# Kernel tuning notes

Measured on AMD Instinct MI355X. Metric: run time of the kernel, lower is better.

Reference implementation:

```python
import jax, jax.numpy as jnp
import numpy as np

TAU = 0.1
EPS_FREQ = 1e-06
EPS_DENOM = 1e-12


def _l2norm(x, eps=1e-12):
    # matches F.normalize(p=2, dim=-1)
    n = jnp.linalg.norm(x, axis=-1, keepdims=True)
    return x / jnp.maximum(n, eps)


def setup_inputs() -> dict:
    key = jax.random.key(0)
    k1, k2, k3, k4, k5 = jax.random.split(key, 5)
    N, D, C = 4096, 128, 64
    return {
        "protos": jax.random.normal(k1, (C, D), dtype=jnp.float32),
        "proj2": jax.random.normal(k2, (N, D), dtype=jnp.float32),
        "target2": jax.random.randint(k3, (N,), 0, C, dtype=jnp.int64),
        "proj3": jax.random.normal(k4, (N, D), dtype=jnp.float32),
        "target3": jax.random.randint(k5, (N,), 0, C, dtype=jnp.int64),
    }


def reference(protos, proj2, target2, proj3, target3):
    feats = _l2norm(jnp.concatenate([proj2, proj3], axis=0))        # [M, D]
    labels = jnp.concatenate([target2, target3], axis=0)             # [M]
    protos_n = _l2norm(protos)                                       # [C, D]
    M = feats.shape[0]
    C = protos_n.shape[0]

    sim = jnp.matmul(feats, feats.T) / TAU                           # [M, M]
    proto_sim = jnp.matmul(feats, protos_n.T) / TAU                  # [M, C]

    eye = jnp.eye(M, dtype=bool)
    exp_sim = jnp.where(eye, 0.0, jnp.exp(sim))                      # diag masked to -inf -> exp 0
    exp_proto = jnp.exp(proto_sim)

    match = labels[:, None] == labels[None, :]                       # [M, M]
    numer_region = jnp.sum(exp_sim * match, axis=1)                  # [M]
    numer_proto = jnp.take_along_axis(exp_proto, labels[:, None], axis=1)[:, 0]
    numer = numer_region + numer_proto

    # bincount(labels ++ arange(C)) == per-class count + 1
    cls_freq = jnp.zeros((C,), dtype=jnp.float32).at[labels].add(1.0) + 1.0 + EPS_FREQ
    feat_w = cls_freq[labels]                                        # [M], per-row weight

    denom_region = jnp.sum(exp_sim, axis=1) / feat_w                 # row-constant weight; diag already 0
    denom_proto = jnp.sum(exp_proto / cls_freq[None, :], axis=1)
    denom = denom_region + denom_proto

    loss = -jnp.log(numer / (denom + EPS_DENOM))
    return jnp.mean(loss)
```

## Files before the change

kernel.cpp:

```cpp
#include <hip/hip_runtime.h>
#include <math.h>
#include <stdint.h>

#define D    128
#define CCLS 64
#define CH   8

typedef _Float16 f16x8 __attribute__((ext_vector_type(8)));
typedef float    f32x4 __attribute__((ext_vector_type(4)));

__device__ __forceinline__ float wave_reduce_sum(float v) {
    #pragma unroll
    for (int off = 32; off > 0; off >>= 1) v += __shfl_xor(v, off, 64);
    return v;
}

__device__ __forceinline__ void gload_lds16(const void* g, void* l) {
    __builtin_amdgcn_global_load_lds(
        (const __attribute__((address_space(1))) uint32_t*)g,
        (__attribute__((address_space(3))) uint32_t*)l, 16, 0, 0);
}
__device__ __forceinline__ void gload_lds4(const void* g, void* l) {
    __builtin_amdgcn_global_load_lds(
        (const __attribute__((address_space(1))) uint32_t*)g,
        (__attribute__((address_space(3))) uint32_t*)l, 4, 0, 0);
}

__global__ void norm_kernel(const float* __restrict__ protos,
                            const float* __restrict__ proj2,
                            const float* __restrict__ proj3,
                            const int* __restrict__ t2, const int* __restrict__ t3,
                            _Float16* __restrict__ ftile, int* __restrict__ labs,
                            float* __restrict__ cls_freq, float* __restrict__ loss_sum,
                            int N, int M) {
    const float SCL = 3.8017368953f;
    int w = threadIdx.x >> 6;
    int lane = threadIdx.x & 63;
    int row = blockIdx.x * (blockDim.x >> 6) + w;
    const int MT = M + 128;

    if (blockIdx.x == 0) {
        __shared__ int h[CCLS];
        int t = threadIdx.x;
        if (t < CCLS) h[t] = 0;
        if (t == 0) loss_sum[0] = 0.f;
        __syncthreads();
        for (int i = t; i < M; i += blockDim.x) {
            int lab = (i < N) ? t2[i] : t3[i - N];
            atomicAdd(&h[lab], 1);
        }
        __syncthreads();
        if (t < CCLS) cls_freq[t] = (float)h[t] + 1.0f + 1e-6f;
    }

    if (row < MT) {
        const float* src = nullptr;
        if (row < M)             src = (row < N) ? proj2 + (size_t)row * D
                                                 : proj3 + (size_t)(row - N) * D;
        else if (row < M + CCLS) src = protos + (size_t)(row - M) * D;
        float2 v = {0.f, 0.f};
        if (src) v = ((const float2*)src)[lane];
        float ss = wave_reduce_sum(v.x * v.x + v.y * v.y);
        float scale = src ? SCL / fmaxf(sqrtf(ss), 1e-12f) : 0.f;
        _Float16 h0 = (_Float16)(v.x * scale), h1 = (_Float16)(v.y * scale);
        int k0 = 2 * lane;
        size_t off = ((size_t)(row >> 4) * 16 + (k0 >> 3)) * 128 + (row & 15) * 8 + (k0 & 7);
        ftile[off] = h0; ftile[off + 1] = h1;
        if (row < M && lane == 0)
            labs[row] = (row < N) ? t2[row] : t3[row - N];
    }
}

__global__ __launch_bounds__(512, 4)
void sim_kernel(const _Float16* __restrict__ ftile,
                const int* __restrict__ labs,
                const float* __restrict__ cls_freq,
                float* __restrict__ nPart, float* __restrict__ dPart,
                float* __restrict__ rp, int M) {
    __shared__ _Float16 sbuf[2][8320];

    const int panel = blockIdx.x;
    const int chunk = blockIdx.y;
    const int t = threadIdx.x;
    const int w = t >> 6, lane = t & 63;
    const int g = lane >> 4, li = lane & 15;
    const int lo = g * 128 + li * 8;
    const int rtA = panel * 8 + w;
    const int nS = (M / 64) / CH;
    const int sBase = chunk * nS;
    const int row = panel * 128 + 16 * w + li;
    const int rl = labs[row];

    f16x8 a[4];
    #pragma unroll
    for (int kt = 0; kt < 4; ++kt)
        a[kt] = *(const f16x8*)(ftile + (size_t)rtA * 2048 + kt * 512 + lo);

    float rn = 0.f, rd = 0.f;

    #define STAGE(buf, s)                                                        \
        {                                                                        \
            const char* bsrc_ = (const char*)ftile + (size_t)(s) * 16384;        \
            char* dst_ = (char*)&sbuf[(buf)][0];                                 \
            _Pragma("unroll")                                                    \
            for (int q = 0; q < 2; ++q) {                                        \
                int j_ = w * 2 + q;                                              \
                gload_lds16(bsrc_ + (size_t)j_ * 1024 + lane * 16,               \
                            dst_ + (size_t)j_ * 1024);                           \
            }                                                                    \
            if (w == 0)                                                          \
                gload_lds4((const char*)labs + (size_t)(s) * 256 + lane * 4,     \
                           dst_ + 16384);                                        \
        }

    STAGE(0, sBase);
    __syncthreads();
    int cur = 0;

    const int diagS = 2 * panel + (w >> 2);
    const int nDiag = w & 3;

    for (int si = 0; si < nS; ++si) {
        const int s = sBase + si;
        if (si + 1 < nS) STAGE(cur ^ 1, sBase + si + 1);

        const _Float16* Bl = &sbuf[cur][0];
        const int* clabL = (const int*)&sbuf[cur][8192];

        f32x4 acc1[4];
        #pragma unroll
        for (int n = 0; n < 4; ++n)
            #pragma unroll
            for (int r = 0; r < 4; ++r) acc1[n][r] = 0.f;

        #pragma unroll
        for (int kt = 0; kt < 4; ++kt) {
            f16x8 b[4];
            #pragma unroll
            for (int n = 0; n < 4; ++n)
                b[n] = *(const f16x8*)(Bl + n * 2048 + kt * 512 + lo);
            #pragma unroll
            for (int n = 0; n < 4; ++n)
                acc1[n] = __builtin_amdgcn_mfma_f32_16x16x32_f16(b[n], a[kt], acc1[n], 0, 0, 0);
        }

        if (s == diagS) {
            #pragma unroll
            for (int n = 0; n < 4; ++n)
                #pragma unroll
                for (int r = 0; r < 4; ++r)
                    acc1[n][r] = (n == nDiag && 4 * g + r == li) ? -1e5f : acc1[n][r];
        }

        #pragma unroll
        for (int n = 0; n < 4; ++n) {
            int4 c4 = *(const int4*)(clabL + 16 * n + 4 * g);
            float e0 = __builtin_amdgcn_exp2f(acc1[n][0]);
            float e1 = __builtin_amdgcn_exp2f(acc1[n][1]);
            float e2 = __builtin_amdgcn_exp2f(acc1[n][2]);
            float e3 = __builtin_amdgcn_exp2f(acc1[n][3]);
            rd += e0 + e1 + e2 + e3;
            rn += (c4.x == rl) ? e0 : 0.f;
            rn += (c4.y == rl) ? e1 : 0.f;
            rn += (c4.z == rl) ? e2 : 0.f;
            rn += (c4.w == rl) ? e3 : 0.f;
        }

        __syncthreads();
        cur ^= 1;
    }

    float rpacc = 0.f;
    if (chunk == 0) {
        const int rbp = M >> 4;
        f32x4 accp[4];
        #pragma unroll
        for (int n = 0; n < 4; ++n)
            #pragma unroll
            for (int r = 0; r < 4; ++r) accp[n][r] = 0.f;
        #pragma unroll
        for (int kt = 0; kt < 4; ++kt) {
            f16x8 b[4];
            #pragma unroll
            for (int n = 0; n < 4; ++n)
                b[n] = *(const f16x8*)(ftile + (size_t)(rbp + n) * 2048 + kt * 512 + lo);
            #pragma unroll
            for (int n = 0; n < 4; ++n)
                accp[n] = __builtin_amdgcn_mfma_f32_16x16x32_f16(b[n], a[kt], accp[n], 0, 0, 0);
        }
        #pragma unroll
        for (int n = 0; n < 4; ++n) {
            f32x4 fr = *(const f32x4*)(cls_freq + 16 * n + 4 * g);
            const int c0 = 16 * n + 4 * g;
            float e0 = __builtin_amdgcn_exp2f(accp[n][0]);
            float e1 = __builtin_amdgcn_exp2f(accp[n][1]);
            float e2 = __builtin_amdgcn_exp2f(accp[n][2]);
            float e3 = __builtin_amdgcn_exp2f(accp[n][3]);
            rpacc += e0 / fr[0] + e1 / fr[1] + e2 / fr[2] + e3 / fr[3];
            rn += (c0 + 0 == rl) ? e0 : 0.f;
            rn += (c0 + 1 == rl) ? e1 : 0.f;
            rn += (c0 + 2 == rl) ? e2 : 0.f;
            rn += (c0 + 3 == rl) ? e3 : 0.f;
        }
    }

    rn += __shfl_xor(rn, 16, 64); rn += __shfl_xor(rn, 32, 64);
    rd += __shfl_xor(rd, 16, 64); rd += __shfl_xor(rd, 32, 64);
    if (chunk == 0) {
        rpacc += __shfl_xor(rpacc, 16, 64); rpacc += __shfl_xor(rpacc, 32, 64);
    }
    if (lane < 16) {
        nPart[(size_t)chunk * M + row] = rn;
        dPart[(size_t)chunk * M + row] = rd;
        if (chunk == 0) rp[row] = rpacc;
    }
}

__global__ void fin_kernel(const int* __restrict__ labs,
                           const float* __restrict__ cls_freq,
                           const float* __restrict__ nPart,
                           const float* __restrict__ dPart,
                           const float* __restrict__ rp,
                           float* __restrict__ loss_sum, int M) {
    int i = blockIdx.x * blockDim.x + threadIdx.x;
    float l = 0.f;
    if (i < M) {
        float rnT = 0.f, rdT = 0.f;
        #pragma unroll
        for (int ch = 0; ch < CH; ++ch) {
            rnT += nPart[(size_t)ch * M + i];
            rdT += dPart[(size_t)ch * M + i];
        }
        float denom = rdT / cls_freq[labs[i]] + rp[i];
        l = logf(denom + 1e-12f) - logf(rnT);
    }
    l = wave_reduce_sum(l);
    __shared__ float ws_[4];
    if ((threadIdx.x & 63) == 0) ws_[threadIdx.x >> 6] = l;
    __syncthreads();
    if (threadIdx.x == 0)
        atomicAdd(loss_sum, ws_[0] + ws_[1] + ws_[2] + ws_[3]);
}

__global__ void out_kernel(const float* __restrict__ loss_sum,
                           float* __restrict__ out, int M) {
    out[0] = loss_sum[0] / (float)M;
}

extern "C" void kernel_launch(void* const* d_in, const int* in_sizes, int n_in,
                              void* d_out, int out_size, void* d_ws, size_t ws_size,
                              hipStream_t stream) {
    const float* protos = (const float*)d_in[0];
    const float* proj2  = (const float*)d_in[1];
    const int*   t2     = (const int*)d_in[2];
    const float* proj3  = (const float*)d_in[3];
    const int*   t3     = (const int*)d_in[4];
    float* out = (float*)d_out;

    const int N = in_sizes[1] / D;
    const int M = 2 * N;
    const int MT = M + 128;

    _Float16* ftile = (_Float16*)d_ws;
    int*   labs     = (int*)(ftile + (size_t)MT * D);
    float* cls_freq = (float*)(labs + M);
    float* nPart    = cls_freq + CCLS;
    float* dPart    = nPart + (size_t)CH * M;
    float* rp       = dPart + (size_t)CH * M;
    float* loss_sum = rp + M;

    norm_kernel<<<(MT + 3) / 4, 256, 0, stream>>>(protos, proj2, proj3, t2, t3,
                                                  ftile, labs, cls_freq, loss_sum, N, M);
    dim3 grid(M / 128, CH);
    sim_kernel<<<grid, 512, 0, stream>>>(ftile, labs, cls_freq, nPart, dPart, rp, M);
    fin_kernel<<<(M + 255) / 256, 256, 0, stream>>>(labs, cls_freq, nPart, dPart, rp,
                                                    loss_sum, M);
    out_kernel<<<1, 1, 0, stream>>>(loss_sum, out, M);
}
```

Before: 39.59 us.

## Give each wave two row tiles, halve block size, double column chunks

Each wave now computes two 16-row A tiles against the same B fragments loaded from LDS, so each LDS read of B feeds twice as many MFMAs. Blocks shrink from 512 to 256 threads, and the column split CH doubles from 8 to 16 so the grid keeps enough blocks. Staging, diagonal masking and the partial-sum writes are adjusted to the new mapping. In exchange, register use per thread rises (two accumulator sets and two A fragment sets), fin_kernel has twice as many partial sums to combine, and there is less parallelism within a block.

```diff
diff --git a/kernel.cpp b/kernel.cpp
--- a/kernel.cpp
+++ b/kernel.cpp
@@ -4,7 +4,7 @@
 
 #define D    128
 #define CCLS 64
-#define CH   8
+#define CH   16
 
 typedef _Float16 f16x8 __attribute__((ext_vector_type(8)));
 typedef float    f32x4 __attribute__((ext_vector_type(4)));
@@ -71,7 +71,7 @@
     }
 }
 
-__global__ __launch_bounds__(512, 4)
+__global__ __launch_bounds__(256, 4)
 void sim_kernel(const _Float16* __restrict__ ftile,
                 const int* __restrict__ labs,
                 const float* __restrict__ cls_freq,
@@ -85,26 +85,30 @@
     const int w = t >> 6, lane = t & 63;
     const int g = lane >> 4, li = lane & 15;
     const int lo = g * 128 + li * 8;
-    const int rtA = panel * 8 + w;
+    const int rtA = panel * 8 + w * 2;
     const int nS = (M / 64) / CH;
     const int sBase = chunk * nS;
-    const int row = panel * 128 + 16 * w + li;
-    const int rl = labs[row];
-
-    f16x8 a[4];
+    const int row0 = panel * 128 + 32 * w + li;
+    const int rl0 = labs[row0];
+    const int rl1 = labs[row0 + 16];
+
+    f16x8 a[2][4];
     #pragma unroll
-    for (int kt = 0; kt < 4; ++kt)
-        a[kt] = *(const f16x8*)(ftile + (size_t)rtA * 2048 + kt * 512 + lo);
-
-    float rn = 0.f, rd = 0.f;
+    for (int m = 0; m < 2; ++m)
+        #pragma unroll
+        for (int kt = 0; kt < 4; ++kt)
+            a[m][kt] = *(const f16x8*)(ftile + (size_t)(rtA + m) * 2048 + kt * 512 + lo);
+
+    float rn[2] = {0.f, 0.f}, rd[2] = {0.f, 0.f};
+    float rpacc[2] = {0.f, 0.f};
 
     #define STAGE(buf, s)                                                        \
         {                                                                        \
             const char* bsrc_ = (const char*)ftile + (size_t)(s) * 16384;        \
             char* dst_ = (char*)&sbuf[(buf)][0];                                 \
             _Pragma("unroll")                                                    \
-            for (int q = 0; q < 2; ++q) {                                        \
-                int j_ = w * 2 + q;                                              \
+            for (int q = 0; q < 4; ++q) {                                        \
+                int j_ = w * 4 + q;                                              \
                 gload_lds16(bsrc_ + (size_t)j_ * 1024 + lane * 16,               \
                             dst_ + (size_t)j_ * 1024);                           \
             }                                                                    \
@@ -117,8 +121,8 @@
     __syncthreads();
     int cur = 0;
 
-    const int diagS = 2 * panel + (w >> 2);
-    const int nDiag = w & 3;
+    const int diagS = 2 * panel + (w >> 1);
+    const int nD0 = 2 * (w & 1);
 
     for (int si = 0; si < nS; ++si) {
         const int s = sBase + si;
@@ -127,11 +131,13 @@
         const _Float16* Bl = &sbuf[cur][0];
         const int* clabL = (const int*)&sbuf[cur][8192];
 
-        f32x4 acc1[4];
-        #pragma unroll
-        for (int n = 0; n < 4; ++n)
-            #pragma unroll
-            for (int r = 0; r < 4; ++r) acc1[n][r] = 0.f;
+        f32x4 acc1[2][4];
+        #pragma unroll
+        for (int m = 0; m < 2; ++m)
+            #pragma unroll
+            for (int n = 0; n < 4; ++n)
+                #pragma unroll
+                for (int r = 0; r < 4; ++r) acc1[m][n][r] = 0.f;
 
         #pragma unroll
         for (int kt = 0; kt < 4; ++kt) {
@@ -140,44 +146,54 @@
             for (int n = 0; n < 4; ++n)
                 b[n] = *(const f16x8*)(Bl + n * 2048 + kt * 512 + lo);
             #pragma unroll
-            for (int n = 0; n < 4; ++n)
-                acc1[n] = __builtin_amdgcn_mfma_f32_16x16x32_f16(b[n], a[kt], acc1[n], 0, 0, 0);
+            for (int m = 0; m < 2; ++m)
+                #pragma unroll
+                for (int n = 0; n < 4; ++n)
+                    acc1[m][n] = __builtin_amdgcn_mfma_f32_16x16x32_f16(b[n], a[m][kt], acc1[m][n], 0, 0, 0);
         }
 
         if (s == diagS) {
             #pragma unroll
-            for (int n = 0; n < 4; ++n)
-                #pragma unroll
-                for (int r = 0; r < 4; ++r)
-                    acc1[n][r] = (n == nDiag && 4 * g + r == li) ? -1e5f : acc1[n][r];
+            for (int m = 0; m < 2; ++m)
+                #pragma unroll
+                for (int n = 0; n < 4; ++n)
+                    #pragma unroll
+                    for (int r = 0; r < 4; ++r)
+                        acc1[m][n][r] = (n == nD0 + m && 4 * g + r == li)
+                                        ? -1e5f : acc1[m][n][r];
         }
 
         #pragma unroll
         for (int n = 0; n < 4; ++n) {
             int4 c4 = *(const int4*)(clabL + 16 * n + 4 * g);
-            float e0 = __builtin_amdgcn_exp2f(acc1[n][0]);
-            float e1 = __builtin_amdgcn_exp2f(acc1[n][1]);
-            float e2 = __builtin_amdgcn_exp2f(acc1[n][2]);
-            float e3 = __builtin_amdgcn_exp2f(acc1[n][3]);
-            rd += e0 + e1 + e2 + e3;
-            rn += (c4.x == rl) ? e0 : 0.f;
-            rn += (c4.y == rl) ? e1 : 0.f;
-            rn += (c4.z == rl) ? e2 : 0.f;
-            rn += (c4.w == rl) ? e3 : 0.f;
+            #pragma unroll
+            for (int m = 0; m < 2; ++m) {
+                float e0 = __builtin_amdgcn_exp2f(acc1[m][n][0]);
+                float e1 = __builtin_amdgcn_exp2f(acc1[m][n][1]);
+                float e2 = __builtin_amdgcn_exp2f(acc1[m][n][2]);
+                float e3 = __builtin_amdgcn_exp2f(acc1[m][n][3]);
+                const int rl = m ? rl1 : rl0;
+                rd[m] += e0 + e1 + e2 + e3;
+                rn[m] += (c4.x == rl) ? e0 : 0.f;
+                rn[m] += (c4.y == rl) ? e1 : 0.f;
+                rn[m] += (c4.z == rl) ? e2 : 0.f;
+                rn[m] += (c4.w == rl) ? e3 : 0.f;
+            }
         }
 
         __syncthreads();
         cur ^= 1;
     }
 
-    float rpacc = 0.f;
     if (chunk == 0) {
         const int rbp = M >> 4;
-        f32x4 accp[4];
-        #pragma unroll
-        for (int n = 0; n < 4; ++n)
-            #pragma unroll
-            for (int r = 0; r < 4; ++r) accp[n][r] = 0.f;
+        f32x4 accp[2][4];
+        #pragma unroll
+        for (int m = 0; m < 2; ++m)
+            #pragma unroll
+            for (int n = 0; n < 4; ++n)
+                #pragma unroll
+                for (int r = 0; r < 4; ++r) accp[m][n][r] = 0.f;
         #pragma unroll
         for (int kt = 0; kt < 4; ++kt) {
             f16x8 b[4];
@@ -185,34 +201,48 @@
             for (int n = 0; n < 4; ++n)
                 b[n] = *(const f16x8*)(ftile + (size_t)(rbp + n) * 2048 + kt * 512 + lo);
             #pragma unroll
-            for (int n = 0; n < 4; ++n)
-                accp[n] = __builtin_amdgcn_mfma_f32_16x16x32_f16(b[n], a[kt], accp[n], 0, 0, 0);
+            for (int m = 0; m < 2; ++m)
+                #pragma unroll
+                for (int n = 0; n < 4; ++n)
+                    accp[m][n] = __builtin_amdgcn_mfma_f32_16x16x32_f16(b[n], a[m][kt], accp[m][n], 0, 0, 0);
         }
         #pragma unroll
         for (int n = 0; n < 4; ++n) {
             f32x4 fr = *(const f32x4*)(cls_freq + 16 * n + 4 * g);
             const int c0 = 16 * n + 4 * g;
-            float e0 = __builtin_amdgcn_exp2f(accp[n][0]);
-            float e1 = __builtin_amdgcn_exp2f(accp[n][1]);
-            float e2 = __builtin_amdgcn_exp2f(accp[n][2]);
-            float e3 = __builtin_amdgcn_exp2f(accp[n][3]);
-            rpacc += e0 / fr[0] + e1 / fr[1] + e2 / fr[2] + e3 / fr[3];
-            rn += (c0 + 0 == rl) ? e0 : 0.f;
-            rn += (c0 + 1 == rl) ? e1 : 0.f;
-            rn += (c0 + 2 == rl) ? e2 : 0.f;
-            rn += (c0 + 3 == rl) ? e3 : 0.f;
-        }
-    }
-
-    rn += __shfl_xor(rn, 16, 64); rn += __shfl_xor(rn, 32, 64);
-    rd += __shfl_xor(rd, 16, 64); rd += __shfl_xor(rd, 32, 64);
-    if (chunk == 0) {
-        rpacc += __shfl_xor(rpacc, 16, 64); rpacc += __shfl_xor(rpacc, 32, 64);
+            #pragma unroll
+            for (int m = 0; m < 2; ++m) {
+                float e0 = __builtin_amdgcn_exp2f(accp[m][n][0]);
+                float e1 = __builtin_amdgcn_exp2f(accp[m][n][1]);
+                float e2 = __builtin_amdgcn_exp2f(accp[m][n][2]);
+                float e3 = __builtin_amdgcn_exp2f(accp[m][n][3]);
+                const int rl = m ? rl1 : rl0;
+                rpacc[m] += e0 / fr[0] + e1 / fr[1] + e2 / fr[2] + e3 / fr[3];
+                rn[m] += (c0 + 0 == rl) ? e0 : 0.f;
+                rn[m] += (c0 + 1 == rl) ? e1 : 0.f;
+                rn[m] += (c0 + 2 == rl) ? e2 : 0.f;
+                rn[m] += (c0 + 3 == rl) ? e3 : 0.f;
+            }
+        }
+    }
+
+    #pragma unroll
+    for (int m = 0; m < 2; ++m) {
+        rn[m] += __shfl_xor(rn[m], 16, 64); rn[m] += __shfl_xor(rn[m], 32, 64);
+        rd[m] += __shfl_xor(rd[m], 16, 64); rd[m] += __shfl_xor(rd[m], 32, 64);
+        if (chunk == 0) {
+            rpacc[m] += __shfl_xor(rpacc[m], 16, 64);
+            rpacc[m] += __shfl_xor(rpacc[m], 32, 64);
+        }
     }
     if (lane < 16) {
-        nPart[(size_t)chunk * M + row] = rn;
-        dPart[(size_t)chunk * M + row] = rd;
-        if (chunk == 0) rp[row] = rpacc;
+        #pragma unroll
+        for (int m = 0; m < 2; ++m) {
+            const int rowm = row0 + 16 * m;
+            nPart[(size_t)chunk * M + rowm] = rn[m];
+            dPart[(size_t)chunk * M + rowm] = rd[m];
+            if (chunk == 0) rp[rowm] = rpacc[m];
+        }
     }
 }
 
@@ -272,7 +302,7 @@
     norm_kernel<<<(MT + 3) / 4, 256, 0, stream>>>(protos, proj2, proj3, t2, t3,
                                                   ftile, labs, cls_freq, loss_sum, N, M);
     dim3 grid(M / 128, CH);
-    sim_kernel<<<grid, 512, 0, stream>>>(ftile, labs, cls_freq, nPart, dPart, rp, M);
+    sim_kernel<<<grid, 256, 0, stream>>>(ftile, labs, cls_freq, nPart, dPart, rp, M);
     fin_kernel<<<(M + 255) / 256, 256, 0, stream>>>(labs, cls_freq, nPart, dPart, rp,
                                                     loss_sum, M);
     out_kernel<<<1, 1, 0, stream>>>(loss_sum, out, M);
```

Result: faster. 38.16 us (-3.6%).
